# Kernel optimization log

Hardware: AMD Instinct MI355X
Metric: run time of the kernel (lower is better)

## Reference

```python
import jax, jax.numpy as jnp
import numpy as np

B, NX, NY, CIN = 4, 128, 128, 64
D, H = 64, 8  # out_channels, nhead
EPS = 1e-5


def setup_inputs() -> dict:
    key = jax.random.key(0)
    ks = jax.random.split(key, 12)
    s_in = 1.0 / np.sqrt(CIN)
    s_hd = 1.0 / np.sqrt(H * D)
    return {
        "v": jax.random.normal(ks[0], (B, NX, NY, CIN), jnp.float32),
        "Wq_w": jax.random.uniform(ks[1], (CIN, H * D), jnp.float32, -s_in, s_in),
        "Wq_b": jax.random.uniform(ks[2], (H * D,), jnp.float32, -s_in, s_in),
        "Wk_w": jax.random.uniform(ks[3], (CIN, H * D), jnp.float32, -s_in, s_in),
        "Wk_b": jax.random.uniform(ks[4], (H * D,), jnp.float32, -s_in, s_in),
        "Wv_w": jax.random.uniform(ks[5], (CIN, H * D), jnp.float32, -s_in, s_in),
        "Wv_b": jax.random.uniform(ks[6], (H * D,), jnp.float32, -s_in, s_in),
        "lnq_g": jnp.ones((H, D), jnp.float32),
        "lnq_b": jnp.zeros((H, D), jnp.float32),
        "lnk_g": jnp.ones((H, D), jnp.float32),
        "lnk_b": jnp.zeros((H, D), jnp.float32),
        "Wo_w": jax.random.uniform(ks[7], (H * D, D), jnp.float32, -s_hd, s_hd),
        "Wo_b": jax.random.uniform(ks[8], (D,), jnp.float32, -s_hd, s_hd),
    }


def _layernorm(x, gamma, beta):
    # x: [b,h,n,d]; gamma/beta: [h,d] (per-head params)
    mu = jnp.mean(x, axis=-1, keepdims=True)
    var = jnp.mean(jnp.square(x - mu), axis=-1, keepdims=True)
    xn = (x - mu) * jax.lax.rsqrt(var + EPS)
    return xn * gamma[None, :, None, :] + beta[None, :, None, :]


def reference(v, Wq_w, Wq_b, Wk_w, Wk_b, Wv_w, Wv_b,
              lnq_g, lnq_b, lnk_g, lnk_b, Wo_w, Wo_b):
    b, nx, ny, _ = v.shape
    n = nx * ny
    vf = v.reshape(b, n, -1)  # [b, n, cin]
    # QKV projections -> [b, h, n, d]
    def proj(w, bias):
        y = vf @ w + bias  # [b, n, h*d]
        return y.reshape(b, n, H, D).transpose(0, 2, 1, 3)
    Q = _layernorm(proj(Wq_w, Wq_b), lnq_g, lnq_b)
    K = _layernorm(proj(Wk_w, Wk_b), lnk_g, lnk_b)
    V = proj(Wv_w, Wv_b)
    # Non-softmax linear attention: (Q K^T) V == Q (K^T V); use O(n d^2) form
    kv = jnp.einsum('bhnd,bhne->bhde', K, V)      # [b,h,d,d]
    attn = jnp.einsum('bhmd,bhde->bhme', Q, kv)   # [b,h,n,d]
    attn = attn.transpose(0, 2, 1, 3).reshape(b, n, H * D)
    out = (attn @ Wo_w + Wo_b) / n
    return out.reshape(b, nx, ny, D)
```

## Files before the change

### kernel.cpp

```cpp
#include <hip/hip_runtime.h>
#include <hip/hip_bf16.h>

typedef __attribute__((ext_vector_type(8))) short bhalf8;
typedef __attribute__((ext_vector_type(4))) float f32x4;

#define MFMA_BF16 __builtin_amdgcn_mfma_f32_16x16x32_bf16

namespace {

constexpr int   NPIX  = 16384;
constexpr int   NCH   = 64;
constexpr int   TILE  = 66 * 64;
constexpr float EPSV  = 1e-5f;
constexpr float INV64 = 1.0f / 64.0f;
constexpr float INV_N = 1.0f / 16384.0f;

__device__ __forceinline__ unsigned short f2bf(float f) {
    unsigned int u = __builtin_bit_cast(unsigned int, f);
    u += 0x7fffu + ((u >> 16) & 1u);
    return (unsigned short)(u >> 16);
}

union B8 { bhalf8 v; unsigned int u[4]; };

__device__ __forceinline__ unsigned int pk2(float a, float b) {
    union { __hip_bfloat162 h; unsigned int u; } x;
    x.h = __float22bfloat162_rn(float2{a, b});
    return x.u;
}

__global__ void kpack(const float* __restrict__ Wk, const float* __restrict__ Wv,
                      const float* __restrict__ Wq,
                      unsigned short* __restrict__ wkpk, unsigned short* __restrict__ wvpk,
                      unsigned short* __restrict__ wqpk, unsigned short* __restrict__ wksumb,
                      float* __restrict__ cbeta)
{
    const int w = blockIdx.x >> 3, h = blockIdx.x & 7, t = threadIdx.x;
    const float* W = (w == 0) ? Wk : (w == 1) ? Wv : Wq;
    unsigned short* dst = (w == 0) ? wkpk : (w == 1) ? wvpk : wqpk;

    if (blockIdx.x == 0) cbeta[t] = 0.f;

#pragma unroll
    for (int i = 0; i < 2; ++i) {
        const int f = t * 2 + i;
        const int nt = (f >> 7) & 3, ks = (f >> 6) & 1, l = f & 63;
        const int g = l >> 4, m = l & 15;
        unsigned short tmp[8];
#pragma unroll
        for (int j = 0; j < 8; ++j)
            tmp[j] = f2bf(W[(size_t)(32 * ks + 8 * g + j) * 512 + h * 64 + 16 * nt + m]);
        unsigned short* d = dst + ((size_t)((h * 4 + nt) * 2 + ks)) * 512 + l * 8;
        *reinterpret_cast<ushort4*>(d)     = make_ushort4(tmp[0], tmp[1], tmp[2], tmp[3]);
        *reinterpret_cast<ushort4*>(d + 4) = make_ushort4(tmp[4], tmp[5], tmp[6], tmp[7]);
    }
    if (w == 0 && t < 64) {
        float s = 0.f;
        const float* row = Wk + (size_t)t * 512 + h * 64;
#pragma unroll
        for (int d = 0; d < 64; ++d) s += row[d];
        wksumb[h * 64 + t] = f2bf(s);
    }
}

__global__ __launch_bounds__(512, 2)
void ka_kv(const float* __restrict__ v,
           const unsigned short* __restrict__ wkpk, const unsigned short* __restrict__ wvpk,
           const unsigned short* __restrict__ wksumb,
           const float* __restrict__ bk, const float* __restrict__ bv,
           float* __restrict__ part)
{
    const int ch = blockIdx.x, b = blockIdx.y;
    const int t = threadIdx.x, h = t >> 6, l = t & 63, g = l >> 4, m16 = l & 15;

    __shared__ uint4 vlds4[2048];
    unsigned short* vlds = reinterpret_cast<unsigned short*>(vlds4);

    const float* vbase = v + ((size_t)b * NPIX + ch * 256) * 64;
#pragma unroll
    for (int i = 0; i < 4; ++i) {
        const int G = t + 512 * i;
        const int s = G >> 8, f = (G >> 6) & 3, ll = G & 63;
        const int mt = f >> 1, ks = f & 1, gg = ll >> 4, mm = ll & 15;
        const float* src = vbase + (size_t)(s * 32 + 16 * mt + mm) * 64 + 32 * ks + 8 * gg;
        const float4 a = *reinterpret_cast<const float4*>(src);
        const float4 c = *reinterpret_cast<const float4*>(src + 4);
        vlds4[G] = uint4{pk2(a.x, a.y), pk2(a.z, a.w), pk2(c.x, c.y), pk2(c.z, c.w)};
    }

    bhalf8 wkB[4][2], wvB[4][2], wks[2];
#pragma unroll
    for (int nt = 0; nt < 4; ++nt)
#pragma unroll
      for (int ks = 0; ks < 2; ++ks) {
          wkB[nt][ks] = *reinterpret_cast<const bhalf8*>(
              wkpk + ((size_t)((h * 4 + nt) * 2 + ks)) * 512 + l * 8);
          wvB[nt][ks] = *reinterpret_cast<const bhalf8*>(
              wvpk + ((size_t)((h * 4 + nt) * 2 + ks)) * 512 + l * 8);
      }
#pragma unroll
    for (int ks = 0; ks < 2; ++ks)
        wks[ks] = *reinterpret_cast<const bhalf8*>(wksumb + h * 64 + 32 * ks + 8 * g);

    float bksum;
    {
        float bl = bk[h * 64 + l];
#pragma unroll
        for (int m = 1; m < 64; m <<= 1) bl += __shfl_xor(bl, m, 64);
        bksum = bl;
    }
    float bkv[4], bvv[4];
#pragma unroll
    for (int nt = 0; nt < 4; ++nt) {
        bkv[nt] = bk[h * 64 + 16 * nt + m16];
        bvv[nt] = bv[h * 64 + 16 * nt + m16];
    }

    f32x4 kv[4][4];
#pragma unroll
    for (int i = 0; i < 4; ++i)
#pragma unroll
      for (int j = 0; j < 4; ++j) kv[i][j] = f32x4{0.f, 0.f, 0.f, 0.f};
    float tl[4] = {0.f, 0.f, 0.f, 0.f};
    float sv[4] = {0.f, 0.f, 0.f, 0.f};

    __syncthreads();

    for (int s = 0; s < 8; ++s) {
        bhalf8 vA[2][2];
#pragma unroll
        for (int mt = 0; mt < 2; ++mt)
#pragma unroll
          for (int ks = 0; ks < 2; ++ks)
            vA[mt][ks] = *reinterpret_cast<const bhalf8*>(
                vlds + ((size_t)(s * 4 + mt * 2 + ks) * 64 + l) * 8);

        f32x4 kq[2][4];
#pragma unroll
        for (int mt = 0; mt < 2; ++mt)
#pragma unroll
          for (int nt = 0; nt < 4; ++nt) {
              f32x4 a = {0.f, 0.f, 0.f, 0.f};
              a = MFMA_BF16(vA[mt][0], wkB[nt][0], a, 0, 0, 0);
              a = MFMA_BF16(vA[mt][1], wkB[nt][1], a, 0, 0, 0);
#pragma unroll
              for (int q = 0; q < 4; ++q) a[q] += bkv[nt];
              kq[mt][nt] = a;
          }
        f32x4 st[2];
#pragma unroll
        for (int mt = 0; mt < 2; ++mt) {
            f32x4 a = {0.f, 0.f, 0.f, 0.f};
            a = MFMA_BF16(vA[mt][0], wks[0], a, 0, 0, 0);
            a = MFMA_BF16(vA[mt][1], wks[1], a, 0, 0, 0);
            st[mt] = a;
        }
        f32x4 s2p[2];
#pragma unroll
        for (int mt = 0; mt < 2; ++mt)
#pragma unroll
          for (int q = 0; q < 4; ++q) {
              float acc = kq[mt][0][q] * kq[mt][0][q];
              acc = fmaf(kq[mt][1][q], kq[mt][1][q], acc);
              acc = fmaf(kq[mt][2][q], kq[mt][2][q], acc);
              acc = fmaf(kq[mt][3][q], kq[mt][3][q], acc);
              s2p[mt][q] = acc;
          }
#pragma unroll
        for (int mt = 0; mt < 2; ++mt)
#pragma unroll
          for (int q = 0; q < 4; ++q) {
              float x = s2p[mt][q];
              x += __shfl_xor(x, 1, 64);
              x += __shfl_xor(x, 2, 64);
              x += __shfl_xor(x, 4, 64);
              x += __shfl_xor(x, 8, 64);
              s2p[mt][q] = x;
          }
        f32x4 rsv[2], cmu[2];
#pragma unroll
        for (int mt = 0; mt < 2; ++mt)
#pragma unroll
          for (int q = 0; q < 4; ++q) {
              const float mu  = (st[mt][q] + bksum) * INV64;
              const float var = s2p[mt][q] * INV64 - mu * mu;
              const float rs  = rsqrtf(fmaxf(var, 0.f) + EPSV);
              rsv[mt][q] = rs;
              cmu[mt][q] = mu * rs;
          }
        B8 ka[4];
#pragma unroll
        for (int MT = 0; MT < 4; ++MT) {
            ka[MT].u[0] = pk2(kq[0][MT][0] * rsv[0][0], kq[0][MT][1] * rsv[0][1]);
            ka[MT].u[1] = pk2(kq[0][MT][2] * rsv[0][2], kq[0][MT][3] * rsv[0][3]);
            ka[MT].u[2] = pk2(kq[1][MT][0] * rsv[1][0], kq[1][MT][1] * rsv[1][1]);
            ka[MT].u[3] = pk2(kq[1][MT][2] * rsv[1][2], kq[1][MT][3] * rsv[1][3]);
        }
        f32x4 vq[2][4];
#pragma unroll
        for (int mt = 0; mt < 2; ++mt)
#pragma unroll
          for (int nt = 0; nt < 4; ++nt) {
              f32x4 a = {0.f, 0.f, 0.f, 0.f};
              a = MFMA_BF16(vA[mt][0], wvB[nt][0], a, 0, 0, 0);
              a = MFMA_BF16(vA[mt][1], wvB[nt][1], a, 0, 0, 0);
#pragma unroll
              for (int q = 0; q < 4; ++q) a[q] += bvv[nt];
              vq[mt][nt] = a;
          }
#pragma unroll
        for (int nt = 0; nt < 4; ++nt) {
            float acc = tl[nt], acc2 = sv[nt];
#pragma unroll
            for (int mt = 0; mt < 2; ++mt)
#pragma unroll
              for (int q = 0; q < 4; ++q) {
                  acc  = fmaf(cmu[mt][q], vq[mt][nt][q], acc);
                  acc2 += vq[mt][nt][q];
              }
            tl[nt] = acc; sv[nt] = acc2;
        }
        B8 vb[4];
#pragma unroll
        for (int NT = 0; NT < 4; ++NT) {
            vb[NT].u[0] = pk2(vq[0][NT][0], vq[0][NT][1]);
            vb[NT].u[1] = pk2(vq[0][NT][2], vq[0][NT][3]);
            vb[NT].u[2] = pk2(vq[1][NT][0], vq[1][NT][1]);
            vb[NT].u[3] = pk2(vq[1][NT][2], vq[1][NT][3]);
        }
#pragma unroll
        for (int MT = 0; MT < 4; ++MT)
#pragma unroll
          for (int NT = 0; NT < 4; ++NT)
              kv[MT][NT] = MFMA_BF16(ka[MT].v, vb[NT].v, kv[MT][NT], 0, 0, 0);
    }

#pragma unroll
    for (int nt = 0; nt < 4; ++nt) {
        float x = tl[nt];
        x += __shfl_xor(x, 16, 64); x += __shfl_xor(x, 32, 64);
        tl[nt] = x;
        float y = sv[nt];
        y += __shfl_xor(y, 16, 64); y += __shfl_xor(y, 32, 64);
        sv[nt] = y;
    }
    float* pdst = part + ((size_t)((b * NCH + ch) * 8 + h)) * TILE;
#pragma unroll
    for (int MT = 0; MT < 4; ++MT)
#pragma unroll
      for (int NT = 0; NT < 4; ++NT)
#pragma unroll
        for (int q = 0; q < 4; ++q)
            pdst[(16 * MT + 4 * g + q) * 64 + 16 * NT + m16] = kv[MT][NT][q];
    if (g == 0) {
#pragma unroll
        for (int nt = 0; nt < 4; ++nt) {
            pdst[64 * 64 + 16 * nt + m16] = tl[nt];
            pdst[65 * 64 + 16 * nt + m16] = sv[nt];
        }
    }
}

__global__ void k2a_reduce(const float* __restrict__ part, float* __restrict__ s2buf)
{
    const int seg = blockIdx.x, bh = blockIdx.y, t = threadIdx.x;
    const int b = bh >> 3, hh = bh & 7;
    const float* base = part + ((size_t)((b * NCH + seg * 8) * 8 + hh)) * TILE;
    float* dst = s2buf + ((size_t)(bh * 8 + seg)) * TILE;
#pragma unroll
    for (int k = 0; k < 5; ++k) {
        const int idx = t + k * 256;
        if (idx < TILE / 4) {
            float4 s = make_float4(0.f, 0.f, 0.f, 0.f);
#pragma unroll
            for (int i = 0; i < 8; ++i) {
                const float4 x = *reinterpret_cast<const float4*>(
                    base + (size_t)i * 8 * TILE + idx * 4);
                s.x += x.x; s.y += x.y; s.z += x.z; s.w += x.w;
            }
            *reinterpret_cast<float4*>(dst + idx * 4) = s;
        }
    }
}

__global__ void k2b_mix(const float* __restrict__ s2buf,
                        const float* __restrict__ lnkg, const float* __restrict__ lnkb,
                        const float* __restrict__ lnqg, const float* __restrict__ lnqb,
                        const float* __restrict__ Wo,   const float* __restrict__ Wob,
                        unsigned short* __restrict__ mpk, float* __restrict__ cbeta)
{
    const int h = blockIdx.x, b = blockIdx.y, t = threadIdx.x;
    __shared__ float kvs[64][65], wos[64][65], mls[64][65], Svs[64], tds[64], us[64];
    const int r = t >> 2, c0 = (t & 3) * 16;
    const float* sb = s2buf + ((size_t)((b * 8 + h) * 8)) * TILE;

    float acc[16];
#pragma unroll
    for (int i = 0; i < 16; ++i) acc[i] = 0.f;
#pragma unroll
    for (int seg = 0; seg < 8; ++seg) {
        const float* src = sb + (size_t)seg * TILE + r * 64 + c0;
#pragma unroll
        for (int q = 0; q < 4; ++q) {
            const float4 x = *reinterpret_cast<const float4*>(src + 4 * q);
            acc[4*q+0] += x.x; acc[4*q+1] += x.y; acc[4*q+2] += x.z; acc[4*q+3] += x.w;
        }
    }
#pragma unroll
    for (int i = 0; i < 16; ++i) kvs[r][c0 + i] = acc[i];

    if (t < 64) {
        float s = 0.f, s2 = 0.f;
#pragma unroll
        for (int seg = 0; seg < 8; ++seg) {
            s  += sb[(size_t)seg * TILE + 64 * 64 + t];
            s2 += sb[(size_t)seg * TILE + 65 * 64 + t];
        }
        tds[t] = s; Svs[t] = s2;
    }
#pragma unroll
    for (int i = 0; i < 16; i += 4) {
        const float4 x = *reinterpret_cast<const float4*>(
            Wo + ((size_t)(h * 64) + r) * 64 + c0 + i);
        wos[r][c0+i] = x.x; wos[r][c0+i+1] = x.y; wos[r][c0+i+2] = x.z; wos[r][c0+i+3] = x.w;
    }
    __syncthreads();
    {
        const float gk = lnkg[h * 64 + r], bk2 = lnkb[h * 64 + r];
#pragma unroll
        for (int i = 0; i < 16; ++i) {
            const int e = c0 + i;
            kvs[r][e] = gk * (kvs[r][e] - tds[e]) + bk2 * Svs[e];
        }
    }
    __syncthreads();
    if (t < 64) {
        float s = 0.f;
        for (int dd = 0; dd < 64; ++dd) s = fmaf(lnqb[h * 64 + dd], kvs[dd][t], s);
        us[t] = s;
    }
    float mrow[16];
#pragma unroll
    for (int i = 0; i < 16; ++i) mrow[i] = 0.f;
    for (int e2 = 0; e2 < 64; ++e2) {
        const float kr = kvs[r][e2];
#pragma unroll
        for (int i = 0; i < 16; ++i) mrow[i] = fmaf(kr, wos[e2][c0 + i], mrow[i]);
    }
    {
        const float gq = lnqg[h * 64 + r] * INV_N;
#pragma unroll
        for (int i = 0; i < 16; ++i) mls[r][c0 + i] = gq * mrow[i];
    }
    __syncthreads();
    if (t < 64) {
        float s = 0.f;
        for (int e2 = 0; e2 < 64; ++e2) s = fmaf(us[e2], wos[e2][t], s);
        atomicAdd(cbeta + b * 64 + t, s * INV_N);
        if (h == 0) atomicAdd(cbeta + b * 64 + t, Wob[t] * INV_N);
    }
#pragma unroll
    for (int i = 0; i < 2; ++i) {
        const int f = t * 2 + i;
        const int nt = (f >> 7) & 3, ks = (f >> 6) & 1, l = f & 63;
        const int g = l >> 4, m = l & 15;
        unsigned short o[8];
#pragma unroll
        for (int j = 0; j < 8; ++j) {
            const int d = 32 * ks + 16 * (j >> 2) + 4 * g + (j & 3);
            o[j] = f2bf(mls[d][16 * nt + m]);
        }
        unsigned short* dd = mpk + ((size_t)((b * 8 + h) * 8 + nt * 2 + ks)) * 512 + l * 8;
        *reinterpret_cast<ushort4*>(dd)     = make_ushort4(o[0], o[1], o[2], o[3]);
        *reinterpret_cast<ushort4*>(dd + 4) = make_ushort4(o[4], o[5], o[6], o[7]);
    }
}

__global__ __launch_bounds__(256, 2)
void k3_out(const float* __restrict__ v,
            const unsigned short* __restrict__ wqpk, const float* __restrict__ bq,
            const unsigned short* __restrict__ mpk,  const float* __restrict__ cbeta,
            float* __restrict__ out)
{
    const int blk = blockIdx.x, b = blockIdx.y;
    const int t = threadIdx.x, w = t >> 6, l = t & 63, g = l >> 4, m16 = l & 15;
    const size_t px0 = (size_t)b * NPIX + blk * 128 + w * 32;

    B8 vB[2][2];
#pragma unroll
    for (int nt = 0; nt < 2; ++nt)
#pragma unroll
      for (int ks = 0; ks < 2; ++ks) {
          const float* src = v + (px0 + 16 * nt + m16) * 64 + 32 * ks + 8 * g;
          const float4 a = *reinterpret_cast<const float4*>(src);
          const float4 c = *reinterpret_cast<const float4*>(src + 4);
          vB[nt][ks].u[0] = pk2(a.x, a.y); vB[nt][ks].u[1] = pk2(a.z, a.w);
          vB[nt][ks].u[2] = pk2(c.x, c.y); vB[nt][ks].u[3] = pk2(c.z, c.w);
      }
    float cbv[4];
#pragma unroll
    for (int nt = 0; nt < 4; ++nt) cbv[nt] = cbeta[b * 64 + 16 * nt + m16];

    f32x4 outa[2][4];
#pragma unroll
    for (int i = 0; i < 2; ++i)
#pragma unroll
      for (int j = 0; j < 4; ++j) outa[i][j] = f32x4{0.f, 0.f, 0.f, 0.f};

#pragma unroll
    for (int h = 0; h < 8; ++h) {
        bhalf8 wqA[4][2], mB[2][4];
#pragma unroll
        for (int mt = 0; mt < 4; ++mt)
#pragma unroll
          for (int ks = 0; ks < 2; ++ks)
            wqA[mt][ks] = *reinterpret_cast<const bhalf8*>(
                wqpk + ((size_t)((h * 4 + mt) * 2 + ks)) * 512 + l * 8);
#pragma unroll
        for (int ks = 0; ks < 2; ++ks)
#pragma unroll
          for (int nt = 0; nt < 4; ++nt)
            mB[ks][nt] = *reinterpret_cast<const bhalf8*>(
                mpk + ((size_t)((b * 8 + h) * 8 + nt * 2 + ks)) * 512 + l * 8);
        float4 bq4[4];
#pragma unroll
        for (int mt = 0; mt < 4; ++mt)
            bq4[mt] = *reinterpret_cast<const float4*>(bq + h * 64 + 16 * mt + 4 * g);

        f32x4 qa[4][2];
#pragma unroll
        for (int mt = 0; mt < 4; ++mt)
#pragma unroll
          for (int nt = 0; nt < 2; ++nt) {
              f32x4 a = {0.f, 0.f, 0.f, 0.f};
              a = MFMA_BF16(wqA[mt][0], vB[nt][0].v, a, 0, 0, 0);
              a = MFMA_BF16(wqA[mt][1], vB[nt][1].v, a, 0, 0, 0);
              a[0] += bq4[mt].x; a[1] += bq4[mt].y;
              a[2] += bq4[mt].z; a[3] += bq4[mt].w;
              qa[mt][nt] = a;
          }
        float mu[2], rs[2];
#pragma unroll
        for (int nt = 0; nt < 2; ++nt) {
            float s1 = 0.f, s2 = 0.f;
#pragma unroll
            for (int mt = 0; mt < 4; ++mt)
#pragma unroll
              for (int q = 0; q < 4; ++q) {
                  const float x = qa[mt][nt][q];
                  s1 += x; s2 = fmaf(x, x, s2);
              }
            s1 += __shfl_xor(s1, 16, 64); s1 += __shfl_xor(s1, 32, 64);
            s2 += __shfl_xor(s2, 16, 64); s2 += __shfl_xor(s2, 32, 64);
            mu[nt] = s1 * INV64;
            rs[nt] = rsqrtf(fmaxf(s2 * INV64 - mu[nt] * mu[nt], 0.f) + EPSV);
        }
        B8 ka[2][2];
#pragma unroll
        for (int MT = 0; MT < 2; ++MT)
#pragma unroll
          for (int ks = 0; ks < 2; ++ks) {
              ka[MT][ks].u[0] = pk2((qa[2*ks+0][MT][0] - mu[MT]) * rs[MT],
                                    (qa[2*ks+0][MT][1] - mu[MT]) * rs[MT]);
              ka[MT][ks].u[1] = pk2((qa[2*ks+0][MT][2] - mu[MT]) * rs[MT],
                                    (qa[2*ks+0][MT][3] - mu[MT]) * rs[MT]);
              ka[MT][ks].u[2] = pk2((qa[2*ks+1][MT][0] - mu[MT]) * rs[MT],
                                    (qa[2*ks+1][MT][1] - mu[MT]) * rs[MT]);
              ka[MT][ks].u[3] = pk2((qa[2*ks+1][MT][2] - mu[MT]) * rs[MT],
                                    (qa[2*ks+1][MT][3] - mu[MT]) * rs[MT]);
          }
#pragma unroll
        for (int MT = 0; MT < 2; ++MT)
#pragma unroll
          for (int nt = 0; nt < 4; ++nt) {
              outa[MT][nt] = MFMA_BF16(ka[MT][0].v, mB[0][nt], outa[MT][nt], 0, 0, 0);
              outa[MT][nt] = MFMA_BF16(ka[MT][1].v, mB[1][nt], outa[MT][nt], 0, 0, 0);
          }
    }

#pragma unroll
    for (int MT = 0; MT < 2; ++MT)
#pragma unroll
      for (int q = 0; q < 4; ++q) {
          float* orow = out + (px0 + 16 * MT + 4 * g + q) * 64;
#pragma unroll
          for (int nt = 0; nt < 4; ++nt)
              orow[16 * nt + m16] = outa[MT][nt][q] + cbv[nt];
      }
}

}

extern "C" void kernel_launch(void* const* d_in, const int* in_sizes, int n_in,
                              void* d_out, int out_size, void* d_ws, size_t ws_size,
                              hipStream_t stream)
{
    const float* v     = (const float*)d_in[0];
    const float* Wq_w  = (const float*)d_in[1];
    const float* Wq_b  = (const float*)d_in[2];
    const float* Wk_w  = (const float*)d_in[3];
    const float* Wk_b  = (const float*)d_in[4];
    const float* Wv_w  = (const float*)d_in[5];
    const float* Wv_b  = (const float*)d_in[6];
    const float* lnq_g = (const float*)d_in[7];
    const float* lnq_b = (const float*)d_in[8];
    const float* lnk_g = (const float*)d_in[9];
    const float* lnk_b = (const float*)d_in[10];
    const float* Wo_w  = (const float*)d_in[11];
    const float* Wo_b  = (const float*)d_in[12];
    float* out = (float*)d_out;

    float* wsf    = (float*)d_ws;
    float* part   = wsf;
    float* s2buf  = part + (size_t)4 * NCH * 8 * TILE;
    float* cbeta  = s2buf + (size_t)32 * 8 * TILE;
    unsigned short* base_s = (unsigned short*)(cbeta + 256);
    unsigned short* wkpk   = base_s;
    unsigned short* wvpk   = base_s + 32768;
    unsigned short* wqpk   = base_s + 65536;
    unsigned short* wksumb = base_s + 98304;
    unsigned short* mpk    = base_s + 98816;

    kpack<<<24, 256, 0, stream>>>(Wk_w, Wv_w, Wq_w, wkpk, wvpk, wqpk, wksumb, cbeta);
    ka_kv<<<dim3(NCH, 4), 512, 0, stream>>>(v, wkpk, wvpk, wksumb, Wk_b, Wv_b, part);
    k2a_reduce<<<dim3(8, 32), 256, 0, stream>>>(part, s2buf);
    k2b_mix<<<dim3(8, 4), 256, 0, stream>>>(s2buf, lnk_g, lnk_b, lnq_g, lnq_b,
                                            Wo_w, Wo_b, mpk, cbeta);
    k3_out<<<dim3(128, 4), 256, 0, stream>>>(v, wqpk, Wq_b, mpk, cbeta, out);
}
```

Before: 161.3 us.

## Fold partial reduction into mix kernel and replace cbeta atomics with per-head buffer

Measured after the change: 185.5 us. 15.0% more time.

```diff
diff --git a/kernel.cpp b/kernel.cpp
--- a/kernel.cpp
+++ b/kernel.cpp
@@ -29,17 +29,14 @@
     return x.u;
 }
 
-__global__ void kpack(const float* __restrict__ Wk, const float* __restrict__ Wv,
-                      const float* __restrict__ Wq,
-                      unsigned short* __restrict__ wkpk, unsigned short* __restrict__ wvpk,
-                      unsigned short* __restrict__ wqpk, unsigned short* __restrict__ wksumb,
-                      float* __restrict__ cbeta)
+__global__ void prep(const float* __restrict__ Wk, const float* __restrict__ Wv,
+                     const float* __restrict__ Wq,
+                     unsigned short* __restrict__ wkpk, unsigned short* __restrict__ wvpk,
+                     unsigned short* __restrict__ wqpk, unsigned short* __restrict__ wksumb)
 {
     const int w = blockIdx.x >> 3, h = blockIdx.x & 7, t = threadIdx.x;
     const float* W = (w == 0) ? Wk : (w == 1) ? Wv : Wq;
     unsigned short* dst = (w == 0) ? wkpk : (w == 1) ? wvpk : wqpk;
-
-    if (blockIdx.x == 0) cbeta[t] = 0.f;
 
 #pragma unroll
     for (int i = 0; i < 2; ++i) {
@@ -140,11 +137,9 @@
         for (int mt = 0; mt < 2; ++mt)
 #pragma unroll
           for (int nt = 0; nt < 4; ++nt) {
-              f32x4 a = {0.f, 0.f, 0.f, 0.f};
+              f32x4 a = {bkv[nt], bkv[nt], bkv[nt], bkv[nt]};
               a = MFMA_BF16(vA[mt][0], wkB[nt][0], a, 0, 0, 0);
               a = MFMA_BF16(vA[mt][1], wkB[nt][1], a, 0, 0, 0);
-#pragma unroll
-              for (int q = 0; q < 4; ++q) a[q] += bkv[nt];
               kq[mt][nt] = a;
           }
         f32x4 st[2];
@@ -201,11 +196,9 @@
         for (int mt = 0; mt < 2; ++mt)
 #pragma unroll
           for (int nt = 0; nt < 4; ++nt) {
-              f32x4 a = {0.f, 0.f, 0.f, 0.f};
+              f32x4 a = {bvv[nt], bvv[nt], bvv[nt], bvv[nt]};
               a = MFMA_BF16(vA[mt][0], wvB[nt][0], a, 0, 0, 0);
               a = MFMA_BF16(vA[mt][1], wvB[nt][1], a, 0, 0, 0);
-#pragma unroll
-              for (int q = 0; q < 4; ++q) a[q] += bvv[nt];
               vq[mt][nt] = a;
           }
 #pragma unroll
@@ -261,60 +254,50 @@
     }
 }
 
-__global__ void k2a_reduce(const float* __restrict__ part, float* __restrict__ s2buf)
-{
-    const int seg = blockIdx.x, bh = blockIdx.y, t = threadIdx.x;
-    const int b = bh >> 3, hh = bh & 7;
-    const float* base = part + ((size_t)((b * NCH + seg * 8) * 8 + hh)) * TILE;
-    float* dst = s2buf + ((size_t)(bh * 8 + seg)) * TILE;
-#pragma unroll
-    for (int k = 0; k < 5; ++k) {
-        const int idx = t + k * 256;
-        if (idx < TILE / 4) {
-            float4 s = make_float4(0.f, 0.f, 0.f, 0.f);
-#pragma unroll
-            for (int i = 0; i < 8; ++i) {
-                const float4 x = *reinterpret_cast<const float4*>(
-                    base + (size_t)i * 8 * TILE + idx * 4);
-                s.x += x.x; s.y += x.y; s.z += x.z; s.w += x.w;
-            }
-            *reinterpret_cast<float4*>(dst + idx * 4) = s;
-        }
-    }
-}
-
-__global__ void k2b_mix(const float* __restrict__ s2buf,
-                        const float* __restrict__ lnkg, const float* __restrict__ lnkb,
-                        const float* __restrict__ lnqg, const float* __restrict__ lnqb,
-                        const float* __restrict__ Wo,   const float* __restrict__ Wob,
-                        unsigned short* __restrict__ mpk, float* __restrict__ cbeta)
+__global__ void mix(const float* __restrict__ part,
+                    const float* __restrict__ lnkg, const float* __restrict__ lnkb,
+                    const float* __restrict__ lnqg, const float* __restrict__ lnqb,
+                    const float* __restrict__ Wo,   const float* __restrict__ Wob,
+                    unsigned short* __restrict__ mpk, float* __restrict__ cbh)
 {
     const int h = blockIdx.x, b = blockIdx.y, t = threadIdx.x;
     __shared__ float kvs[64][65], wos[64][65], mls[64][65], Svs[64], tds[64], us[64];
     const int r = t >> 2, c0 = (t & 3) * 16;
-    const float* sb = s2buf + ((size_t)((b * 8 + h) * 8)) * TILE;
+    const float* pb = part + ((size_t)(b * NCH * 8 + h)) * TILE;
 
     float acc[16];
 #pragma unroll
     for (int i = 0; i < 16; ++i) acc[i] = 0.f;
-#pragma unroll
-    for (int seg = 0; seg < 8; ++seg) {
-        const float* src = sb + (size_t)seg * TILE + r * 64 + c0;
-#pragma unroll
-        for (int q = 0; q < 4; ++q) {
-            const float4 x = *reinterpret_cast<const float4*>(src + 4 * q);
-            acc[4*q+0] += x.x; acc[4*q+1] += x.y; acc[4*q+2] += x.z; acc[4*q+3] += x.w;
-        }
+    for (int s8 = 0; s8 < 8; ++s8) {
+        float tmp[16];
+#pragma unroll
+        for (int i = 0; i < 16; ++i) tmp[i] = 0.f;
+#pragma unroll
+        for (int i8 = 0; i8 < 8; ++i8) {
+            const float* src = pb + (size_t)(s8 * 8 + i8) * 8 * TILE + r * 64 + c0;
+#pragma unroll
+            for (int q = 0; q < 4; ++q) {
+                const float4 x = *reinterpret_cast<const float4*>(src + 4 * q);
+                tmp[4*q+0] += x.x; tmp[4*q+1] += x.y; tmp[4*q+2] += x.z; tmp[4*q+3] += x.w;
+            }
+        }
+#pragma unroll
+        for (int i = 0; i < 16; ++i) acc[i] += tmp[i];
     }
 #pragma unroll
     for (int i = 0; i < 16; ++i) kvs[r][c0 + i] = acc[i];
 
     if (t < 64) {
         float s = 0.f, s2 = 0.f;
-#pragma unroll
-        for (int seg = 0; seg < 8; ++seg) {
-            s  += sb[(size_t)seg * TILE + 64 * 64 + t];
-            s2 += sb[(size_t)seg * TILE + 65 * 64 + t];
+        for (int s8 = 0; s8 < 8; ++s8) {
+            float a1 = 0.f, a2 = 0.f;
+#pragma unroll
+            for (int i8 = 0; i8 < 8; ++i8) {
+                const float* src = pb + (size_t)(s8 * 8 + i8) * 8 * TILE;
+                a1 += src[64 * 64 + t];
+                a2 += src[65 * 64 + t];
+            }
+            s += a1; s2 += a2;
         }
         tds[t] = s; Svs[t] = s2;
     }
@@ -356,8 +339,7 @@
     if (t < 64) {
         float s = 0.f;
         for (int e2 = 0; e2 < 64; ++e2) s = fmaf(us[e2], wos[e2][t], s);
-        atomicAdd(cbeta + b * 64 + t, s * INV_N);
-        if (h == 0) atomicAdd(cbeta + b * 64 + t, Wob[t] * INV_N);
+        cbh[(size_t)(b * 8 + h) * 64 + t] = s * INV_N;
     }
 #pragma unroll
     for (int i = 0; i < 2; ++i) {
@@ -379,8 +361,8 @@
 __global__ __launch_bounds__(256, 2)
 void k3_out(const float* __restrict__ v,
             const unsigned short* __restrict__ wqpk, const float* __restrict__ bq,
-            const unsigned short* __restrict__ mpk,  const float* __restrict__ cbeta,
-            float* __restrict__ out)
+            const unsigned short* __restrict__ mpk,  const float* __restrict__ cbh,
+            const float* __restrict__ Wob, float* __restrict__ out)
 {
     const int blk = blockIdx.x, b = blockIdx.y;
     const int t = threadIdx.x, w = t >> 6, l = t & 63, g = l >> 4, m16 = l & 15;
@@ -399,7 +381,13 @@
       }
     float cbv[4];
 #pragma unroll
-    for (int nt = 0; nt < 4; ++nt) cbv[nt] = cbeta[b * 64 + 16 * nt + m16];
+    for (int nt = 0; nt < 4; ++nt) {
+        const int e = 16 * nt + m16;
+        float s = Wob[e] * INV_N;
+#pragma unroll
+        for (int h = 0; h < 8; ++h) s += cbh[(size_t)(b * 8 + h) * 64 + e];
+        cbv[nt] = s;
+    }
 
     f32x4 outa[2][4];
 #pragma unroll
@@ -432,11 +420,9 @@
         for (int mt = 0; mt < 4; ++mt)
 #pragma unroll
           for (int nt = 0; nt < 2; ++nt) {
-              f32x4 a = {0.f, 0.f, 0.f, 0.f};
+              f32x4 a = {bq4[mt].x, bq4[mt].y, bq4[mt].z, bq4[mt].w};
               a = MFMA_BF16(wqA[mt][0], vB[nt][0].v, a, 0, 0, 0);
               a = MFMA_BF16(wqA[mt][1], vB[nt][1].v, a, 0, 0, 0);
-              a[0] += bq4[mt].x; a[1] += bq4[mt].y;
-              a[2] += bq4[mt].z; a[3] += bq4[mt].w;
               qa[mt][nt] = a;
           }
         float mu[2], rs[2];
@@ -512,19 +498,17 @@
 
     float* wsf    = (float*)d_ws;
     float* part   = wsf;
-    float* s2buf  = part + (size_t)4 * NCH * 8 * TILE;
-    float* cbeta  = s2buf + (size_t)32 * 8 * TILE;
-    unsigned short* base_s = (unsigned short*)(cbeta + 256);
+    float* cbh    = part + (size_t)4 * NCH * 8 * TILE;
+    unsigned short* base_s = (unsigned short*)(cbh + 2048);
     unsigned short* wkpk   = base_s;
     unsigned short* wvpk   = base_s + 32768;
     unsigned short* wqpk   = base_s + 65536;
     unsigned short* wksumb = base_s + 98304;
     unsigned short* mpk    = base_s + 98816;
 
-    kpack<<<24, 256, 0, stream>>>(Wk_w, Wv_w, Wq_w, wkpk, wvpk, wqpk, wksumb, cbeta);
+    prep<<<24, 256, 0, stream>>>(Wk_w, Wv_w, Wq_w, wkpk, wvpk, wqpk, wksumb);
     ka_kv<<<dim3(NCH, 4), 512, 0, stream>>>(v, wkpk, wvpk, wksumb, Wk_b, Wv_b, part);
-    k2a_reduce<<<dim3(8, 32), 256, 0, stream>>>(part, s2buf);
-    k2b_mix<<<dim3(8, 4), 256, 0, stream>>>(s2buf, lnk_g, lnk_b, lnq_g, lnq_b,
-                                            Wo_w, Wo_b, mpk, cbeta);
-    k3_out<<<dim3(128, 4), 256, 0, stream>>>(v, wqpk, Wq_b, mpk, cbeta, out);
-}
+    mix<<<dim3(8, 4), 256, 0, stream>>>(part, lnk_g, lnk_b, lnq_g, lnq_b,
+                                        Wo_w, Wo_b, mpk, cbh);
+    k3_out<<<dim3(128, 4), 256, 0, stream>>>(v, wqpk, Wq_b, mpk, cbh, Wo_b, out);
+}
```
